# Performance work log

Measured on AMD Instinct MI355X. Metric: run time of the kernel, lower is better.

## Reference

```python
import jax, jax.numpy as jnp
import numpy as np

N, E = 50000, 800000
IN, OUT, ED = 64, 128, 16
L_CONV, CLS, L_CLS = 4, 256, 2
NUM_MOLS = 2000
BN_INV = 1.0 / np.sqrt(1.0 + 1e-5).astype(np.float32)  # BN eval: running_mean=0, running_var=1


def leaky(v):
    return jnp.where(v > 0, v, 0.01 * v)


def gine_conv(x, src, dst, edge_attr, eW, eb, W, b, gamma, beta):
    # PyG GINEConv (eps=0): nn(x + sum_j relu(x_j + lin_e(edge_attr)))
    e = edge_attr @ eW + eb                       # [E, d_in]
    msg = jax.nn.relu(x[src] + e)                 # [E, d_in]
    agg = jax.ops.segment_sum(msg, dst, num_segments=N)  # [N, d_in]
    h = (x + agg) @ W + b                         # [N, OUT]
    h = gamma * (h * BN_INV) + beta               # BatchNorm1d (eval)
    return leaky(h)                               # LeakyReLU inside nn (Dropout=identity)


def setup_inputs() -> dict:
    key = jax.random.key(0)
    ks = jax.random.split(key, 24)
    s = 0.05
    inp = {
        "x": jax.random.normal(ks[0], (N, IN), jnp.float32),
        "edge_index": jax.random.randint(ks[1], (2, E), 0, N, jnp.int32),
        "edge_attr": jax.random.normal(ks[2], (E, ED), jnp.float32),
        "batch": jnp.sort(jax.random.randint(ks[3], (N,), 0, NUM_MOLS, jnp.int32)),
        "conv1_W": jax.random.normal(ks[4], (IN, OUT), jnp.float32) * s,
        "conv1_b": jnp.zeros((OUT,), jnp.float32),
        "conv1_gamma": jnp.ones((OUT,), jnp.float32),
        "conv1_beta": jnp.zeros((OUT,), jnp.float32),
        "conv1_eW": jax.random.normal(ks[5], (ED, IN), jnp.float32) * s,
        "conv1_eb": jnp.zeros((IN,), jnp.float32),
        "conv_W": jax.random.normal(ks[6], (L_CONV, OUT, OUT), jnp.float32) * s,
        "conv_b": jnp.zeros((L_CONV, OUT), jnp.float32),
        "conv_gamma": jnp.ones((L_CONV, OUT), jnp.float32),
        "conv_beta": jnp.zeros((L_CONV, OUT), jnp.float32),
        "conv_eW": jax.random.normal(ks[7], (L_CONV, ED, OUT), jnp.float32) * s,
        "conv_eb": jnp.zeros((L_CONV, OUT), jnp.float32),
        "cls1_W": jax.random.normal(ks[8], (OUT * (L_CONV + 1), CLS), jnp.float32) * s,
        "cls1_b": jnp.zeros((CLS,), jnp.float32),
        "cls_W": jax.random.normal(ks[9], (L_CLS, CLS, CLS), jnp.float32) * s,
        "cls_b": jnp.zeros((L_CLS, CLS), jnp.float32),
        "final_W": jax.random.normal(ks[10], (CLS, 1), jnp.float32) * s,
        "final_b": jnp.zeros((1,), jnp.float32),
    }
    return inp


def reference(x, edge_index, edge_attr, batch,
              conv1_W, conv1_b, conv1_gamma, conv1_beta, conv1_eW, conv1_eb,
              conv_W, conv_b, conv_gamma, conv_beta, conv_eW, conv_eb,
              cls1_W, cls1_b, cls_W, cls_b, final_W, final_b):
    src, dst = edge_index[0], edge_index[1]
    h = gine_conv(x, src, dst, edge_attr, conv1_eW, conv1_eb,
                  conv1_W, conv1_b, conv1_gamma, conv1_beta)
    h = leaky(h)  # outer LeakyReLU in forward (note: conv1 output not in hs)
    hs = []
    for i in range(conv_W.shape[0]):
        h = gine_conv(h, src, dst, edge_attr, conv_eW[i], conv_eb[i],
                      conv_W[i], conv_b[i], conv_gamma[i], conv_beta[i])
        h = leaky(h)
        hs.append(h)
    h_pool = jax.ops.segment_sum(h, batch, num_segments=NUM_MOLS)  # global_add_pool
    h_pool_nodes = h_pool[batch]  # repeat_interleave by per-mol counts (batch sorted)
    h = jnp.concatenate(hs + [h_pool_nodes], axis=1)  # [N, OUT*(L_CONV+1)]
    h = h @ cls1_W + cls1_b  # no activation after classifier1 (as in source)
    for i in range(cls_W.shape[0]):
        h = leaky(h @ cls_W[i] + cls_b[i])
    return jax.nn.sigmoid(h @ final_W + final_b)  # [N, 1]
```

## Files before the change

### kernel.cpp

```cpp
#include <hip/hip_runtime.h>
#include <hip/hip_bf16.h>
#include <math.h>

#define N_NODES 50000
#define N_EDGES 800000
#define N_MOLS  2000
#define EPB     128

static constexpr float BN_INV_F = 0.9999950000374997f;

enum { ACT_NONE = 0, ACT_LEAKY = 1, ACT_BN_DL = 2 };

typedef float f32x4 __attribute__((ext_vector_type(4)));
typedef short bf16x8 __attribute__((ext_vector_type(8)));

static __device__ __forceinline__ float b2f(short s) {
    unsigned u = ((unsigned)(unsigned short)s) << 16;
    return __builtin_bit_cast(float, u);
}
static __device__ __forceinline__ short f2bs(float v) {
    return __builtin_bit_cast(short, __float2bfloat16(v));
}


__global__ void hist_kernel(const int* __restrict__ ei, int* __restrict__ cnt) {
    int e = blockIdx.x * 256 + threadIdx.x;
    if (e < N_EDGES) atomicAdd(&cnt[ei[N_EDGES + e]], 1);
}

__global__ __launch_bounds__(1024) void scan1_kernel(const int* __restrict__ cnt,
                                                     int* __restrict__ incl,
                                                     int* __restrict__ bsum) {
    __shared__ int sd[1024];
    int i = blockIdx.x * 1024 + threadIdx.x;
    int v = (i < N_NODES) ? cnt[i] : 0;
    sd[threadIdx.x] = v;
    __syncthreads();
    for (int off = 1; off < 1024; off <<= 1) {
        int t = (threadIdx.x >= off) ? sd[threadIdx.x - off] : 0;
        __syncthreads();
        sd[threadIdx.x] += t;
        __syncthreads();
    }
    incl[i] = sd[threadIdx.x];
    if (threadIdx.x == 1023) bsum[blockIdx.x] = sd[1023];
}

__global__ void scan2_kernel(const int* __restrict__ bsum, int* __restrict__ bex, int nblk) {
    if (threadIdx.x == 0) {
        int run = 0;
        for (int b = 0; b < nblk; ++b) { bex[b] = run; run += bsum[b]; }
    }
}

__global__ __launch_bounds__(1024) void scan3_kernel(const int* __restrict__ cnt,
                                                     const int* __restrict__ incl,
                                                     const int* __restrict__ bex,
                                                     int* __restrict__ cursor) {
    int i = blockIdx.x * 1024 + threadIdx.x;
    if (i < N_NODES) cursor[i] = bex[blockIdx.x] + incl[i] - cnt[i];
}

__global__ void scatter_kernel(const int* __restrict__ ei, int* __restrict__ cursor,
                               const float* __restrict__ ea,
                               int* __restrict__ srcs, int* __restrict__ dsts,
                               __hip_bfloat16* __restrict__ eas) {
    int e = blockIdx.x * 256 + threadIdx.x;
    if (e < N_EDGES) {
        int d = ei[N_EDGES + e];
        int pos = atomicAdd(&cursor[d], 1);
        srcs[pos] = ei[e];
        dsts[pos] = d;
        const f32x4* s4 = (const f32x4*)(ea + (size_t)e * 16);
        f32x4 a0 = s4[0], a1 = s4[1], a2 = s4[2], a3 = s4[3];
        bf16x8 lo, hi;
#pragma unroll
        for (int j = 0; j < 4; ++j) {
            lo[j] = f2bs(a0[j]); lo[4 + j] = f2bs(a1[j]);
            hi[j] = f2bs(a2[j]); hi[4 + j] = f2bs(a3[j]);
        }
        bf16x8* d8 = (bf16x8*)(eas + (size_t)pos * 16);
        d8[0] = lo; d8[1] = hi;
    }
}


__global__ __launch_bounds__(256) void cvt_all_kernel(
        const float* __restrict__ c1W, const float* __restrict__ cW,
        const float* __restrict__ cls1W, const float* __restrict__ clsW,
        const float* __restrict__ c1eW, const float* __restrict__ ceW,
        __hip_bfloat16* __restrict__ wt1, __hip_bfloat16* __restrict__ wtc,
        __hip_bfloat16* __restrict__ wtcls1, __hip_bfloat16* __restrict__ wtcls,
        __hip_bfloat16* __restrict__ ewt1, __hip_bfloat16* __restrict__ ewtc) {
    int o = blockIdx.x * 256 + threadIdx.x;
    auto cvt = [](const float* s, __hip_bfloat16* d, int K, int Nc, int off) {
        int n = off / K, k = off - n * K;
        d[off] = __float2bfloat16(s[(size_t)k * Nc + n]);
    };
    if (o < 8192) cvt(c1W, wt1, 64, 128, o);
    else if (o < 73728)  { int s = o - 8192;   int i = s >> 14, off = s & 16383;
        cvt(cW + i * 16384, wtc + i * 16384, 128, 128, off); }
    else if (o < 237568) cvt(cls1W, wtcls1, 640, 256, o - 73728);
    else if (o < 368640) { int s = o - 237568; int i = s >> 16, off = s & 65535;
        cvt(clsW + i * 65536, wtcls + i * 65536, 256, 256, off); }
    else if (o < 369664) cvt(c1eW, ewt1, 16, 64, o - 368640);
    else if (o < 377856) { int s = o - 369664; int i = s >> 11, off = s & 2047;
        cvt(ceW + i * 2048, ewtc + i * 2048, 16, 128, off); }
}


template<int D, bool F32IN>
__global__ __launch_bounds__(256) void edge_mfma_kernel(
        const void* __restrict__ hin_, int ld,
        const __hip_bfloat16* __restrict__ eas,
        const int* __restrict__ srcs,
        const int* __restrict__ dsts,
        const __hip_bfloat16* __restrict__ eWt,
        const float* __restrict__ eb,
        float* __restrict__ t32) {
    constexpr int SP = D + 4;
    constexpr int NCT = D / 16;
    constexpr int GROUPS = 256 / D;
    constexpr int EPG = EPB / GROUPS;
    __shared__ __hip_bfloat16 e_lds[EPB * SP];
    const int tid = threadIdx.x;
    const int wid = tid >> 6, lane = tid & 63;
    const int lrow = lane & 15;
    const int lkg = lane >> 4;
    const bool hiK = lkg >= 2;
    const int lko = (lkg & 1) * 8;
    const int p0 = blockIdx.x * EPB;

    bf16x8 bfrag[NCT];
#pragma unroll
    for (int ct = 0; ct < NCT; ++ct) {
        bf16x8 bv = *reinterpret_cast<const bf16x8*>(&eWt[(ct * 16 + lrow) * 16 + lko]);
        if (hiK) bv = (bf16x8){0, 0, 0, 0, 0, 0, 0, 0};
        bfrag[ct] = bv;
    }
#pragma unroll
    for (int et = 0; et < 2; ++et) {
        const int erow = (wid * 2 + et) * 16;
        bf16x8 av = *reinterpret_cast<const bf16x8*>(
            &eas[(size_t)(p0 + erow + lrow) * 16 + lko]);
        if (hiK) av = (bf16x8){0, 0, 0, 0, 0, 0, 0, 0};
        const int r0 = erow + lkg * 4;
#pragma unroll
        for (int ct = 0; ct < NCT; ++ct) {
            f32x4 c = (f32x4){0.f, 0.f, 0.f, 0.f};
            c = __builtin_amdgcn_mfma_f32_16x16x32_bf16(av, bfrag[ct], c, 0, 0, 0);
            const int col = ct * 16 + lrow;
            const float bi = eb[col];
#pragma unroll
            for (int r = 0; r < 4; ++r)
                e_lds[(r0 + r) * SP + col] = __float2bfloat16(c[r] + bi);
        }
    }
    __syncthreads();

    const float* hf = (const float*)hin_;
    const __hip_bfloat16* hb = (const __hip_bfloat16*)hin_;
    const int g = tid / D;
    const int f = tid - g * D;
    const int q0 = g * EPG;
    int cur = dsts[p0 + q0];
    float acc = 0.f;
    for (int q = q0; q < q0 + EPG; q += 8) {
        int s[8], d[8];
#pragma unroll
        for (int j = 0; j < 8; ++j) { s[j] = srcs[p0 + q + j]; d[j] = dsts[p0 + q + j]; }
        float h[8];
#pragma unroll
        for (int j = 0; j < 8; ++j)
            h[j] = F32IN ? hf[(size_t)s[j] * ld + f]
                         : __bfloat162float(hb[(size_t)s[j] * ld + f]);
        float e[8];
#pragma unroll
        for (int j = 0; j < 8; ++j)
            e[j] = __bfloat162float(e_lds[(q + j) * SP + f]);
#pragma unroll
        for (int j = 0; j < 8; ++j) {
            if (d[j] != cur) {
                atomicAdd(&t32[(size_t)cur * D + f], acc);
                acc = 0.f; cur = d[j];
            }
            acc += fmaxf(h[j] + e[j], 0.f);
        }
    }
    atomicAdd(&t32[(size_t)cur * D + f], acc);
}


template<int DIN, int DOUT, int ACT, int SELF>
__global__ __launch_bounds__(256) void mfma_lin_kernel(
        const void* __restrict__ A_, int lda,
        const float* __restrict__ t32,
        const __hip_bfloat16* __restrict__ Wt,
        const float* __restrict__ bias,
        const float* __restrict__ gamma,
        const float* __restrict__ beta,
        __hip_bfloat16* __restrict__ C, int ldc) {
    constexpr int NT = DOUT / 32;
    constexpr int NKS = DIN / 32;
    const int wid = threadIdx.x >> 6, lane = threadIdx.x & 63;
    const int wr = wid >> 1, wc = wid & 1;
    const int row_base = blockIdx.x * 32 + wr * 16;
    const int col_base = wc * NT * 16;
    const int lrow = lane & 15;
    const int lk = (lane >> 4) * 8;

    int arow = row_base + lrow;
    arow = arow < N_NODES ? arow : N_NODES - 1;

    bf16x8 a[NKS];
    if constexpr (SELF == 0) {
        const __hip_bfloat16* Ab = (const __hip_bfloat16*)A_;
#pragma unroll
        for (int ks = 0; ks < NKS; ++ks)
            a[ks] = *reinterpret_cast<const bf16x8*>(&Ab[(size_t)arow * lda + ks * 32 + lk]);
    } else if constexpr (SELF == 1) {
        const float* Af = (const float*)A_;
        f32x4 t0[NKS], t1[NKS], h0[NKS], h1[NKS];
#pragma unroll
        for (int ks = 0; ks < NKS; ++ks) {
            const int kc = ks * 32 + lk;
            t0[ks] = *(const f32x4*)&t32[(size_t)arow * DIN + kc];
            t1[ks] = *(const f32x4*)&t32[(size_t)arow * DIN + kc + 4];
            h0[ks] = *(const f32x4*)&Af[(size_t)arow * lda + kc];
            h1[ks] = *(const f32x4*)&Af[(size_t)arow * lda + kc + 4];
        }
#pragma unroll
        for (int ks = 0; ks < NKS; ++ks)
#pragma unroll
            for (int j = 0; j < 4; ++j) {
                a[ks][j]     = f2bs(t0[ks][j] + h0[ks][j]);
                a[ks][4 + j] = f2bs(t1[ks][j] + h1[ks][j]);
            }
    } else {
        const __hip_bfloat16* Ab = (const __hip_bfloat16*)A_;
        f32x4 t0[NKS], t1[NKS];
        bf16x8 hv[NKS];
#pragma unroll
        for (int ks = 0; ks < NKS; ++ks) {
            const int kc = ks * 32 + lk;
            t0[ks] = *(const f32x4*)&t32[(size_t)arow * DIN + kc];
            t1[ks] = *(const f32x4*)&t32[(size_t)arow * DIN + kc + 4];
            hv[ks] = *reinterpret_cast<const bf16x8*>(&Ab[(size_t)arow * lda + kc]);
        }
#pragma unroll
        for (int ks = 0; ks < NKS; ++ks)
#pragma unroll
            for (int j = 0; j < 4; ++j) {
                a[ks][j]     = f2bs(t0[ks][j] + b2f(hv[ks][j]));
                a[ks][4 + j] = f2bs(t1[ks][j] + b2f(hv[ks][4 + j]));
            }
    }

    f32x4 acc[NT];
#pragma unroll
    for (int nt = 0; nt < NT; ++nt) acc[nt] = (f32x4){0.f, 0.f, 0.f, 0.f};
#pragma unroll
    for (int ks = 0; ks < NKS; ++ks) {
        const int kc = ks * 32 + lk;
#pragma unroll
        for (int nt = 0; nt < NT; ++nt) {
            bf16x8 b = *reinterpret_cast<const bf16x8*>(
                &Wt[(size_t)(col_base + nt * 16 + lrow) * DIN + kc]);
            acc[nt] = __builtin_amdgcn_mfma_f32_16x16x32_bf16(a[ks], b, acc[nt], 0, 0, 0);
        }
    }

    const int r0 = row_base + (lane >> 4) * 4;
#pragma unroll
    for (int nt = 0; nt < NT; ++nt) {
        int c = col_base + nt * 16 + lrow;
        float bi = bias[c];
        float ga = (ACT == ACT_BN_DL) ? gamma[c] : 0.f;
        float be = (ACT == ACT_BN_DL) ? beta[c] : 0.f;
#pragma unroll
        for (int r = 0; r < 4; ++r) {
            int row = r0 + r;
            if (row < N_NODES) {
                float v = acc[nt][r] + bi;
                if (ACT == ACT_BN_DL) {
                    v = ga * (v * BN_INV_F) + be;
                    v = v > 0.f ? v : 1e-4f * v;
                } else if (ACT == ACT_LEAKY) {
                    v = v > 0.f ? v : 0.01f * v;
                }
                C[(size_t)row * ldc + c] = __float2bfloat16(v);
            }
        }
    }
}


__global__ void pool_add_kernel(const __hip_bfloat16* __restrict__ concat,
                                const int* __restrict__ batch,
                                float* __restrict__ pool) {
    int idx = blockIdx.x * 256 + threadIdx.x;
    if (idx >= N_NODES * 128) return;
    int n = idx >> 7, f = idx & 127;
    atomicAdd(&pool[batch[n] * 128 + f],
              __bfloat162float(concat[(size_t)n * 640 + 384 + f]));
}

__global__ void pool_gather_kernel(__hip_bfloat16* __restrict__ concat,
                                   const int* __restrict__ batch,
                                   const float* __restrict__ pool) {
    int idx = blockIdx.x * 256 + threadIdx.x;
    if (idx >= N_NODES * 128) return;
    int n = idx >> 7, f = idx & 127;
    concat[(size_t)n * 640 + 512 + f] = __float2bfloat16(pool[batch[n] * 128 + f]);
}


__global__ __launch_bounds__(256) void final_kernel(const __hip_bfloat16* __restrict__ A,
                                                    const float* __restrict__ fW,
                                                    const float* __restrict__ fb,
                                                    float* __restrict__ out) {
    int wave = threadIdx.x >> 6;
    int lane = threadIdx.x & 63;
    int row = blockIdx.x * 4 + wave;
    const __hip_bfloat16* ar = A + (size_t)row * 256;
    float p = 0.f;
#pragma unroll
    for (int i = 0; i < 4; ++i) {
        int k = lane + i * 64;
        p += __bfloat162float(ar[k]) * fW[k];
    }
#pragma unroll
    for (int off = 32; off >= 1; off >>= 1) p += __shfl_xor(p, off, 64);
    if (lane == 0) out[row] = 1.f / (1.f + expf(-(p + fb[0])));
}


extern "C" void kernel_launch(void* const* d_in, const int* in_sizes, int n_in,
                              void* d_out, int out_size, void* d_ws, size_t ws_size,
                              hipStream_t stream) {
    const float* x     = (const float*)d_in[0];
    const int*   ei    = (const int*)d_in[1];
    const float* ea    = (const float*)d_in[2];
    const int*   batch = (const int*)d_in[3];
    const float* c1W   = (const float*)d_in[4];
    const float* c1b   = (const float*)d_in[5];
    const float* c1g   = (const float*)d_in[6];
    const float* c1be  = (const float*)d_in[7];
    const float* c1eW  = (const float*)d_in[8];
    const float* c1eb  = (const float*)d_in[9];
    const float* cW    = (const float*)d_in[10];
    const float* cb    = (const float*)d_in[11];
    const float* cg    = (const float*)d_in[12];
    const float* cbe   = (const float*)d_in[13];
    const float* ceW   = (const float*)d_in[14];
    const float* ceb   = (const float*)d_in[15];
    const float* cls1W = (const float*)d_in[16];
    const float* cls1b = (const float*)d_in[17];
    const float* clsW  = (const float*)d_in[18];
    const float* clsb  = (const float*)d_in[19];
    const float* fW    = (const float*)d_in[20];
    const float* fb    = (const float*)d_in[21];
    float* out = (float*)d_out;

    char* ws = (char*)d_ws;
    size_t off = 0;
    auto alloc = [&](size_t bytes) {
        void* p = ws + off;
        off += (bytes + 255) & ~(size_t)255;
        return p;
    };
    const int NBLK = (N_NODES + 1023) / 1024;
    int*   srcs   = (int*)alloc((size_t)N_EDGES * 4);
    int*   dsts   = (int*)alloc((size_t)N_EDGES * 4);
    int*   cursor = (int*)alloc((size_t)N_NODES * 4);
    int*   cnt    = (int*)alloc((size_t)N_NODES * 4);
    int*   incl   = (int*)alloc((size_t)NBLK * 1024 * 4);
    int*   bsum   = (int*)alloc((size_t)NBLK * 4);
    int*   bex    = (int*)alloc((size_t)NBLK * 4);
    __hip_bfloat16* eas = (__hip_bfloat16*)alloc((size_t)N_EDGES * 16 * 2);
    float* t32    = (float*)alloc((size_t)N_NODES * 128 * 4);
    __hip_bfloat16* h1     = (__hip_bfloat16*)alloc((size_t)N_NODES * 128 * 2);
    float*          pool   = (float*)alloc((size_t)N_MOLS * 128 * 4);
    __hip_bfloat16* concat = (__hip_bfloat16*)alloc((size_t)N_NODES * 640 * 2);
    __hip_bfloat16* clsA   = (__hip_bfloat16*)alloc((size_t)N_NODES * 256 * 2);
    __hip_bfloat16* wt1    = (__hip_bfloat16*)alloc((size_t)128 * 64 * 2);
    __hip_bfloat16* wtc    = (__hip_bfloat16*)alloc((size_t)4 * 128 * 128 * 2);
    __hip_bfloat16* wtcls1 = (__hip_bfloat16*)alloc((size_t)256 * 640 * 2);
    __hip_bfloat16* wtcls  = (__hip_bfloat16*)alloc((size_t)2 * 256 * 256 * 2);
    __hip_bfloat16* ewt1   = (__hip_bfloat16*)alloc((size_t)64 * 16 * 2);
    __hip_bfloat16* ewtc   = (__hip_bfloat16*)alloc((size_t)4 * 128 * 16 * 2);
    __hip_bfloat16* clsB   = concat;

    hipMemsetAsync(cnt, 0, (size_t)N_NODES * 4, stream);
    hipMemsetAsync(pool, 0, (size_t)N_MOLS * 128 * 4, stream);

    hist_kernel<<<(N_EDGES + 255) / 256, 256, 0, stream>>>(ei, cnt);
    scan1_kernel<<<NBLK, 1024, 0, stream>>>(cnt, incl, bsum);
    scan2_kernel<<<1, 64, 0, stream>>>(bsum, bex, NBLK);
    scan3_kernel<<<NBLK, 1024, 0, stream>>>(cnt, incl, bex, cursor);
    scatter_kernel<<<(N_EDGES + 255) / 256, 256, 0, stream>>>(ei, cursor, ea, srcs, dsts, eas);

    cvt_all_kernel<<<(377856 + 255) / 256, 256, 0, stream>>>(
        c1W, cW, cls1W, clsW, c1eW, ceW, wt1, wtc, wtcls1, wtcls, ewt1, ewtc);

    const int NEB = N_EDGES / EPB;
    const int GRID_LIN = (N_NODES + 31) / 32;

    hipMemsetAsync(t32, 0, (size_t)N_NODES * 64 * 4, stream);
    edge_mfma_kernel<64, true><<<NEB, 256, 0, stream>>>(
        x, 64, eas, srcs, dsts, ewt1, c1eb, t32);
    mfma_lin_kernel<64, 128, ACT_BN_DL, 1><<<GRID_LIN, 256, 0, stream>>>(
        x, 64, t32, wt1, c1b, c1g, c1be, h1, 128);

    for (int i = 0; i < 4; ++i) {
        const void* hin = (i == 0) ? (const void*)h1 : (const void*)(concat + (size_t)(i - 1) * 128);
        int ld = (i == 0) ? 128 : 640;
        hipMemsetAsync(t32, 0, (size_t)N_NODES * 128 * 4, stream);
        edge_mfma_kernel<128, false><<<NEB, 256, 0, stream>>>(
            hin, ld, eas, srcs, dsts, ewtc + (size_t)i * 2048, ceb + (size_t)i * 128, t32);
        mfma_lin_kernel<128, 128, ACT_BN_DL, 2><<<GRID_LIN, 256, 0, stream>>>(
            hin, ld, t32, wtc + (size_t)i * 16384, cb + i * 128,
            cg + i * 128, cbe + i * 128, concat + (size_t)i * 128, 640);
    }

    pool_add_kernel<<<(N_NODES * 128 + 255) / 256, 256, 0, stream>>>(concat, batch, pool);
    pool_gather_kernel<<<(N_NODES * 128 + 255) / 256, 256, 0, stream>>>(concat, batch, pool);

    mfma_lin_kernel<640, 256, ACT_NONE, 0><<<GRID_LIN, 256, 0, stream>>>(
        concat, 640, nullptr, wtcls1, cls1b, nullptr, nullptr, clsA, 256);
    mfma_lin_kernel<256, 256, ACT_LEAKY, 0><<<GRID_LIN, 256, 0, stream>>>(
        clsA, 256, nullptr, wtcls, clsb, nullptr, nullptr, clsB, 256);
    mfma_lin_kernel<256, 256, ACT_LEAKY, 0><<<GRID_LIN, 256, 0, stream>>>(
        clsB, 256, nullptr, wtcls + 256 * 256, clsb + 256, nullptr, nullptr, clsA, 256);
    final_kernel<<<N_NODES / 4, 256, 0, stream>>>(clsA, fW, fb, out);
}
```

Before: 1.068 ms.

## Stage weight tiles in swizzled LDS and tile dense layers over 2D grid

The dense MFMA kernel now gives each block a 64x64 output tile over a 2D grid. Each block stages the matching weight slice into XOR-swizzled shared memory, and the K dimension is processed in chunks of up to 128. Before, every wave read the weights straight from global memory with a strided per-lane pattern, and each block computed all output columns for 32 rows. The goal is to share weight loads across waves and raise occupancy through smaller register footprints and launch bounds. The cost is extra barriers, LDS traffic, and A-row tiles that are reloaded once per column block.

```diff
diff --git a/kernel.cpp b/kernel.cpp
--- a/kernel.cpp
+++ b/kernel.cpp
@@ -192,7 +192,7 @@
 
 
 template<int DIN, int DOUT, int ACT, int SELF>
-__global__ __launch_bounds__(256) void mfma_lin_kernel(
+__global__ __launch_bounds__(256, 4) void mfma_lin_kernel(
         const void* __restrict__ A_, int lda,
         const float* __restrict__ t32,
         const __hip_bfloat16* __restrict__ Wt,
@@ -200,80 +200,114 @@
         const float* __restrict__ gamma,
         const float* __restrict__ beta,
         __hip_bfloat16* __restrict__ C, int ldc) {
-    constexpr int NT = DOUT / 32;
-    constexpr int NKS = DIN / 32;
-    const int wid = threadIdx.x >> 6, lane = threadIdx.x & 63;
-    const int wr = wid >> 1, wc = wid & 1;
-    const int row_base = blockIdx.x * 32 + wr * 16;
-    const int col_base = wc * NT * 16;
+    constexpr int KC   = (DIN < 128) ? DIN : 128;
+    constexpr int NCH  = DIN / KC;
+    constexpr int NKSC = KC / 32;
+    constexpr int CPR  = KC / 8;
+    constexpr int TC   = (64 * CPR) / 256;
+    static_assert(SELF == 0 || NCH == 1, "SELF modes need single chunk");
+    __shared__ __align__(16) short Bs[64 * KC];
+
+    const int tid = threadIdx.x;
+    const int wid = tid >> 6, lane = tid & 63;
     const int lrow = lane & 15;
-    const int lk = (lane >> 4) * 8;
-
+    const int g = lane >> 4;
+    const int lk = g * 8;
+    const int row_base = blockIdx.x * 64 + wid * 16;
+    const int col0 = blockIdx.y * 64;
     int arow = row_base + lrow;
     arow = arow < N_NODES ? arow : N_NODES - 1;
 
-    bf16x8 a[NKS];
-    if constexpr (SELF == 0) {
-        const __hip_bfloat16* Ab = (const __hip_bfloat16*)A_;
-#pragma unroll
-        for (int ks = 0; ks < NKS; ++ks)
-            a[ks] = *reinterpret_cast<const bf16x8*>(&Ab[(size_t)arow * lda + ks * 32 + lk]);
-    } else if constexpr (SELF == 1) {
-        const float* Af = (const float*)A_;
-        f32x4 t0[NKS], t1[NKS], h0[NKS], h1[NKS];
-#pragma unroll
-        for (int ks = 0; ks < NKS; ++ks) {
-            const int kc = ks * 32 + lk;
-            t0[ks] = *(const f32x4*)&t32[(size_t)arow * DIN + kc];
-            t1[ks] = *(const f32x4*)&t32[(size_t)arow * DIN + kc + 4];
-            h0[ks] = *(const f32x4*)&Af[(size_t)arow * lda + kc];
-            h1[ks] = *(const f32x4*)&Af[(size_t)arow * lda + kc + 4];
-        }
-#pragma unroll
-        for (int ks = 0; ks < NKS; ++ks)
-#pragma unroll
-            for (int j = 0; j < 4; ++j) {
-                a[ks][j]     = f2bs(t0[ks][j] + h0[ks][j]);
-                a[ks][4 + j] = f2bs(t1[ks][j] + h1[ks][j]);
+    const int srow = tid >> 2;
+    const int sc0 = (tid & 3) * TC;
+    char* BsB = (char*)Bs;
+
+    f32x4 acc[4];
+#pragma unroll
+    for (int nt = 0; nt < 4; ++nt) acc[nt] = (f32x4){0.f, 0.f, 0.f, 0.f};
+
+    for (int ch = 0; ch < NCH; ++ch) {
+        const int kc0 = ch * KC;
+
+        bf16x8 a[NKSC];
+        f32x4 t0[NKSC], t1[NKSC];
+        bf16x8 hv[NKSC];
+        f32x4 h0[NKSC], h1[NKSC];
+        if constexpr (SELF == 0) {
+            const __hip_bfloat16* Ab = (const __hip_bfloat16*)A_;
+#pragma unroll
+            for (int ks = 0; ks < NKSC; ++ks)
+                a[ks] = *reinterpret_cast<const bf16x8*>(
+                    &Ab[(size_t)arow * lda + kc0 + ks * 32 + lk]);
+        } else if constexpr (SELF == 1) {
+            const float* Af = (const float*)A_;
+#pragma unroll
+            for (int ks = 0; ks < NKSC; ++ks) {
+                const int kc = ks * 32 + lk;
+                t0[ks] = *(const f32x4*)&t32[(size_t)arow * DIN + kc];
+                t1[ks] = *(const f32x4*)&t32[(size_t)arow * DIN + kc + 4];
+                h0[ks] = *(const f32x4*)&Af[(size_t)arow * lda + kc];
+                h1[ks] = *(const f32x4*)&Af[(size_t)arow * lda + kc + 4];
             }
-    } else {
-        const __hip_bfloat16* Ab = (const __hip_bfloat16*)A_;
-        f32x4 t0[NKS], t1[NKS];
-        bf16x8 hv[NKS];
-#pragma unroll
-        for (int ks = 0; ks < NKS; ++ks) {
-            const int kc = ks * 32 + lk;
-            t0[ks] = *(const f32x4*)&t32[(size_t)arow * DIN + kc];
-            t1[ks] = *(const f32x4*)&t32[(size_t)arow * DIN + kc + 4];
-            hv[ks] = *reinterpret_cast<const bf16x8*>(&Ab[(size_t)arow * lda + kc]);
-        }
-#pragma unroll
-        for (int ks = 0; ks < NKS; ++ks)
-#pragma unroll
-            for (int j = 0; j < 4; ++j) {
-                a[ks][j]     = f2bs(t0[ks][j] + b2f(hv[ks][j]));
-                a[ks][4 + j] = f2bs(t1[ks][j] + b2f(hv[ks][4 + j]));
+        } else {
+            const __hip_bfloat16* Ab = (const __hip_bfloat16*)A_;
+#pragma unroll
+            for (int ks = 0; ks < NKSC; ++ks) {
+                const int kc = ks * 32 + lk;
+                t0[ks] = *(const f32x4*)&t32[(size_t)arow * DIN + kc];
+                t1[ks] = *(const f32x4*)&t32[(size_t)arow * DIN + kc + 4];
+                hv[ks] = *reinterpret_cast<const bf16x8*>(&Ab[(size_t)arow * lda + kc]);
             }
-    }
-
-    f32x4 acc[NT];
-#pragma unroll
-    for (int nt = 0; nt < NT; ++nt) acc[nt] = (f32x4){0.f, 0.f, 0.f, 0.f};
-#pragma unroll
-    for (int ks = 0; ks < NKS; ++ks) {
-        const int kc = ks * 32 + lk;
-#pragma unroll
-        for (int nt = 0; nt < NT; ++nt) {
-            bf16x8 b = *reinterpret_cast<const bf16x8*>(
-                &Wt[(size_t)(col_base + nt * 16 + lrow) * DIN + kc]);
-            acc[nt] = __builtin_amdgcn_mfma_f32_16x16x32_bf16(a[ks], b, acc[nt], 0, 0, 0);
-        }
-    }
-
-    const int r0 = row_base + (lane >> 4) * 4;
-#pragma unroll
-    for (int nt = 0; nt < NT; ++nt) {
-        int c = col_base + nt * 16 + lrow;
+        }
+
+        bf16x8 breg[TC];
+#pragma unroll
+        for (int j = 0; j < TC; ++j)
+            breg[j] = *reinterpret_cast<const bf16x8*>(
+                &Wt[(size_t)(col0 + srow) * DIN + kc0 + (sc0 + j) * 8]);
+#pragma unroll
+        for (int j = 0; j < TC; ++j) {
+            const int c = sc0 + j;
+            *(bf16x8*)(BsB + srow * (KC * 2) + ((c ^ (srow & 7)) * 16)) = breg[j];
+        }
+        __syncthreads();
+
+        if constexpr (SELF == 1) {
+#pragma unroll
+            for (int ks = 0; ks < NKSC; ++ks)
+#pragma unroll
+                for (int j = 0; j < 4; ++j) {
+                    a[ks][j]     = f2bs(t0[ks][j] + h0[ks][j]);
+                    a[ks][4 + j] = f2bs(t1[ks][j] + h1[ks][j]);
+                }
+        } else if constexpr (SELF == 2) {
+#pragma unroll
+            for (int ks = 0; ks < NKSC; ++ks)
+#pragma unroll
+                for (int j = 0; j < 4; ++j) {
+                    a[ks][j]     = f2bs(t0[ks][j] + b2f(hv[ks][j]));
+                    a[ks][4 + j] = f2bs(t1[ks][j] + b2f(hv[ks][4 + j]));
+                }
+        }
+
+#pragma unroll
+        for (int ks = 0; ks < NKSC; ++ks) {
+#pragma unroll
+            for (int nt = 0; nt < 4; ++nt) {
+                const int brow = nt * 16 + lrow;
+                const int c = ks * 4 + g;
+                bf16x8 b = *(const bf16x8*)(
+                    BsB + brow * (KC * 2) + ((c ^ (brow & 7)) * 16));
+                acc[nt] = __builtin_amdgcn_mfma_f32_16x16x32_bf16(a[ks], b, acc[nt], 0, 0, 0);
+            }
+        }
+        if (ch + 1 < NCH) __syncthreads();
+    }
+
+    const int r0 = row_base + g * 4;
+#pragma unroll
+    for (int nt = 0; nt < 4; ++nt) {
+        int c = col0 + nt * 16 + lrow;
         float bi = bias[c];
         float ga = (ACT == ACT_BN_DL) ? gamma[c] : 0.f;
         float be = (ACT == ACT_BN_DL) ? beta[c] : 0.f;
@@ -404,12 +438,12 @@
         c1W, cW, cls1W, clsW, c1eW, ceW, wt1, wtc, wtcls1, wtcls, ewt1, ewtc);
 
     const int NEB = N_EDGES / EPB;
-    const int GRID_LIN = (N_NODES + 31) / 32;
+    const int GR = (N_NODES + 63) / 64;
 
     hipMemsetAsync(t32, 0, (size_t)N_NODES * 64 * 4, stream);
     edge_mfma_kernel<64, true><<<NEB, 256, 0, stream>>>(
         x, 64, eas, srcs, dsts, ewt1, c1eb, t32);
-    mfma_lin_kernel<64, 128, ACT_BN_DL, 1><<<GRID_LIN, 256, 0, stream>>>(
+    mfma_lin_kernel<64, 128, ACT_BN_DL, 1><<<dim3(GR, 2), 256, 0, stream>>>(
         x, 64, t32, wt1, c1b, c1g, c1be, h1, 128);
 
     for (int i = 0; i < 4; ++i) {
@@ -418,7 +452,7 @@
         hipMemsetAsync(t32, 0, (size_t)N_NODES * 128 * 4, stream);
         edge_mfma_kernel<128, false><<<NEB, 256, 0, stream>>>(
             hin, ld, eas, srcs, dsts, ewtc + (size_t)i * 2048, ceb + (size_t)i * 128, t32);
-        mfma_lin_kernel<128, 128, ACT_BN_DL, 2><<<GRID_LIN, 256, 0, stream>>>(
+        mfma_lin_kernel<128, 128, ACT_BN_DL, 2><<<dim3(GR, 2), 256, 0, stream>>>(
             hin, ld, t32, wtc + (size_t)i * 16384, cb + i * 128,
             cg + i * 128, cbe + i * 128, concat + (size_t)i * 128, 640);
     }
@@ -426,11 +460,11 @@
     pool_add_kernel<<<(N_NODES * 128 + 255) / 256, 256, 0, stream>>>(concat, batch, pool);
     pool_gather_kernel<<<(N_NODES * 128 + 255) / 256, 256, 0, stream>>>(concat, batch, pool);
 
-    mfma_lin_kernel<640, 256, ACT_NONE, 0><<<GRID_LIN, 256, 0, stream>>>(
+    mfma_lin_kernel<640, 256, ACT_NONE, 0><<<dim3(GR, 4), 256, 0, stream>>>(
         concat, 640, nullptr, wtcls1, cls1b, nullptr, nullptr, clsA, 256);
-    mfma_lin_kernel<256, 256, ACT_LEAKY, 0><<<GRID_LIN, 256, 0, stream>>>(
+    mfma_lin_kernel<256, 256, ACT_LEAKY, 0><<<dim3(GR, 4), 256, 0, stream>>>(
         clsA, 256, nullptr, wtcls, clsb, nullptr, nullptr, clsB, 256);
-    mfma_lin_kernel<256, 256, ACT_LEAKY, 0><<<GRID_LIN, 256, 0, stream>>>(
+    mfma_lin_kernel<256, 256, ACT_LEAKY, 0><<<dim3(GR, 4), 256, 0, stream>>>(
         clsB, 256, nullptr, wtcls + 256 * 256, clsb + 256, nullptr, nullptr, clsA, 256);
     final_kernel<<<N_NODES / 4, 256, 0, stream>>>(clsA, fW, fb, out);
 }
```

New measurement: 855.4 us. -19.9%, faster.
